# Kernel tuning notes

Measured on AMD Instinct MI355X. Metric: run time of the kernel, lower is better.

The kernel has to match this reference:

```python
import jax, jax.numpy as jnp
import numpy as np

B, N, D_IMG = 64, 196, 2048
T = 32
V, E, H, A = 32000, 512, 1024, 256
PAD_ID = 0


def setup_inputs() -> dict:
    key = jax.random.key(0)
    ks = jax.random.split(key, 16)
    s = lambda *sh: 1.0 / np.sqrt(sh[-1])
    img_seq = jax.random.normal(ks[0], (B, N, D_IMG), dtype=jnp.float32)
    tokens_in = jax.random.randint(ks[1], (B, T), 0, V, dtype=jnp.int64)
    embed = jax.random.normal(ks[2], (V, E), dtype=jnp.float32) * 0.02
    embed = embed.at[PAD_ID].set(0.0)  # padding_idx row is zero
    W_head1 = jax.random.normal(ks[3], (E, E + D_IMG), dtype=jnp.float32) * s(E + D_IMG)
    W_ih = jax.random.normal(ks[4], (4 * H, E), dtype=jnp.float32) * s(H)
    W_hh = jax.random.normal(ks[5], (4 * H, H), dtype=jnp.float32) * s(H)
    b_ih = jax.random.normal(ks[6], (4 * H,), dtype=jnp.float32) * s(H)
    b_hh = jax.random.normal(ks[7], (4 * H,), dtype=jnp.float32) * s(H)
    W_head = jax.random.normal(ks[8], (V, H), dtype=jnp.float32) * s(H)
    W_img = jax.random.normal(ks[9], (A, D_IMG), dtype=jnp.float32) * s(D_IMG)
    W_hid = jax.random.normal(ks[10], (A, H), dtype=jnp.float32) * s(H)
    w_score = jax.random.normal(ks[11], (A,), dtype=jnp.float32) * s(A)
    W_h0 = jax.random.normal(ks[12], (H, D_IMG), dtype=jnp.float32) * s(D_IMG)
    b_h0 = jax.random.normal(ks[13], (H,), dtype=jnp.float32) * s(D_IMG)
    W_c0 = jax.random.normal(ks[14], (H, D_IMG), dtype=jnp.float32) * s(D_IMG)
    b_c0 = jax.random.normal(ks[15], (H,), dtype=jnp.float32) * s(D_IMG)
    return dict(img_seq=img_seq, tokens_in=tokens_in, embed=embed, W_head1=W_head1,
                W_ih=W_ih, W_hh=W_hh, b_ih=b_ih, b_hh=b_hh, W_head=W_head,
                W_img=W_img, W_hid=W_hid, w_score=w_score,
                W_h0=W_h0, b_h0=b_h0, W_c0=W_c0, b_c0=b_c0)


def _decode(img_seq, tokens_in, embed, W_head1, W_ih, W_hh, b_ih, b_hh,
            W_head, W_img, W_hid, w_score, W_h0, b_h0, W_c0, b_c0):
    g = img_seq.mean(axis=1)                              # [B, D]
    h = jnp.tanh(g @ W_h0.T + b_h0)                       # [B, H]
    c = jnp.tanh(g @ W_c0.T + b_c0)                       # [B, H]
    # image projection is time-invariant: hoist out of the loop
    proj_img = jnp.einsum('bnd,ad->bna', img_seq, W_img)  # [B, N, A]
    emb_all = embed[tokens_in]                            # [B, T, E]

    def step(carry, emb_t):
        h, c = carry
        # additive attention
        proj_h = h @ W_hid.T                              # [B, A]
        scores = jnp.einsum('bna,a->bn', jnp.tanh(proj_img + proj_h[:, None, :]), w_score)
        weights = jax.nn.softmax(scores, axis=-1)         # [B, N]
        ctx = jnp.einsum('bn,bnd->bd', weights, img_seq)  # [B, D]
        x = jnp.concatenate([emb_t, ctx], axis=-1) @ W_head1.T  # [B, E]
        # LSTMCell (PyTorch gate order: i, f, g, o)
        gates = x @ W_ih.T + b_ih + h @ W_hh.T + b_hh     # [B, 4H]
        i, f, gg, o = jnp.split(gates, 4, axis=-1)
        c_new = jax.nn.sigmoid(f) * c + jax.nn.sigmoid(i) * jnp.tanh(gg)
        h_new = jax.nn.sigmoid(o) * jnp.tanh(c_new)
        logits = h_new @ W_head.T                         # [B, V]
        return (h_new, c_new), logits

    _, ys = jax.lax.scan(step, (h, c), jnp.swapaxes(emb_all, 0, 1))  # ys: [T, B, V]
    return jnp.swapaxes(ys, 0, 1)                         # [B, T, V]


def reference(img_seq, tokens_in, embed, W_head1, W_ih, W_hh, b_ih, b_hh,
              W_head, W_img, W_hid, w_score, W_h0, b_h0, W_c0, b_c0):
    return _decode(img_seq, tokens_in, embed, W_head1, W_ih, W_hh, b_ih, b_hh,
                   W_head, W_img, W_hid, w_score, W_h0, b_h0, W_c0, b_c0)
```

## Files before the change

kernel.cpp:

```cpp
#include <hip/hip_runtime.h>
#include <stdint.h>

typedef unsigned short u16;
typedef __bf16 bf16x8 __attribute__((ext_vector_type(8)));
typedef float f32x4 __attribute__((ext_vector_type(4)));

#define DEV static __device__ __forceinline__

DEV u16 f2bu(float f) {
    union { float f; unsigned u; } v; v.f = f;
    unsigned r = v.u + 0x7FFFu + ((v.u >> 16) & 1u);
    return (u16)(r >> 16);
}
DEV float b2f(u16 b) {
    union { unsigned u; float f; } v; v.u = ((unsigned)b) << 16;
    return v.f;
}
DEV float fast_tanh(float x) {
    float e = __expf(2.f * x);
    return 1.f - __fdividef(2.f, e + 1.f);
}
DEV float fast_sig(float x) {
    return __fdividef(1.f, 1.f + __expf(-x));
}
DEV void gload_lds(const u16* g, u16* l) {
    __builtin_amdgcn_global_load_lds((const __attribute__((address_space(1))) void*)g,
                                     (__attribute__((address_space(3))) void*)l, 16, 0, 0);
}

template<bool A_F32, bool B_F32, bool B_KXN, bool OUT_BF16, bool BIAS>
__global__ __launch_bounds__(256) void gemm128(
    const void* __restrict__ Ap, int lda,
    const void* __restrict__ Bp, int ldb,
    void* __restrict__ Cp, int ldc,
    const float* __restrict__ bias, int K)
{
    __shared__ u16 As[128 * 40];
    __shared__ u16 Bs[128 * 40];
    const int tid = threadIdx.x;
    const int lane = tid & 63, wave = tid >> 6;
    const int wr = wave >> 1, wc = wave & 1;
    const int m0 = blockIdx.y * 128, n0 = blockIdx.x * 128;

    f32x4 acc[4][4];
#pragma unroll
    for (int m = 0; m < 4; ++m)
#pragma unroll
        for (int n = 0; n < 4; ++n)
            acc[m][n] = (f32x4){0.f, 0.f, 0.f, 0.f};

    for (int k0 = 0; k0 < K; k0 += 32) {
        __syncthreads();
        if (A_F32) {
            const float* A = (const float*)Ap;
#pragma unroll
            for (int i = 0; i < 4; ++i) {
                int c = tid + i * 256;
                int row = c >> 3, kc = (c & 7) * 4;
                float4 v = *(const float4*)&A[(size_t)(m0 + row) * lda + k0 + kc];
                ushort4 o; o.x = f2bu(v.x); o.y = f2bu(v.y); o.z = f2bu(v.z); o.w = f2bu(v.w);
                *(ushort4*)&As[row * 40 + kc] = o;
            }
        } else {
            const u16* A = (const u16*)Ap;
#pragma unroll
            for (int i = 0; i < 2; ++i) {
                int c = tid + i * 256;
                int row = c >> 2, kc = (c & 3) * 8;
                *(int4*)&As[row * 40 + kc] = *(const int4*)&A[(size_t)(m0 + row) * lda + k0 + kc];
            }
        }
        if (B_KXN) {
            const float* B = (const float*)Bp;
#pragma unroll
            for (int i = 0; i < 4; ++i) {
                int c = tid + i * 256;
                int kk = c >> 5, nc = (c & 31) * 4;
                float4 v = *(const float4*)&B[(size_t)(k0 + kk) * ldb + n0 + nc];
                Bs[(nc + 0) * 40 + kk] = f2bu(v.x);
                Bs[(nc + 1) * 40 + kk] = f2bu(v.y);
                Bs[(nc + 2) * 40 + kk] = f2bu(v.z);
                Bs[(nc + 3) * 40 + kk] = f2bu(v.w);
            }
        } else if (B_F32) {
            const float* B = (const float*)Bp;
#pragma unroll
            for (int i = 0; i < 4; ++i) {
                int c = tid + i * 256;
                int row = c >> 3, kc = (c & 7) * 4;
                float4 v = *(const float4*)&B[(size_t)(n0 + row) * ldb + k0 + kc];
                ushort4 o; o.x = f2bu(v.x); o.y = f2bu(v.y); o.z = f2bu(v.z); o.w = f2bu(v.w);
                *(ushort4*)&Bs[row * 40 + kc] = o;
            }
        } else {
            const u16* B = (const u16*)Bp;
#pragma unroll
            for (int i = 0; i < 2; ++i) {
                int c = tid + i * 256;
                int row = c >> 2, kc = (c & 3) * 8;
                *(int4*)&Bs[row * 40 + kc] = *(const int4*)&B[(size_t)(n0 + row) * ldb + k0 + kc];
            }
        }
        __syncthreads();
        const int fr = lane & 15, kq = (lane >> 4) * 8;
        bf16x8 af[4], bq[4];
#pragma unroll
        for (int m = 0; m < 4; ++m)
            af[m] = *(const bf16x8*)&As[(wr * 64 + m * 16 + fr) * 40 + kq];
#pragma unroll
        for (int n = 0; n < 4; ++n)
            bq[n] = *(const bf16x8*)&Bs[(wc * 64 + n * 16 + fr) * 40 + kq];
#pragma unroll
        for (int m = 0; m < 4; ++m)
#pragma unroll
            for (int n = 0; n < 4; ++n)
                acc[m][n] = __builtin_amdgcn_mfma_f32_16x16x32_bf16(af[m], bq[n], acc[m][n], 0, 0, 0);
    }
    const int fr = lane & 15, rq = (lane >> 4) * 4;
#pragma unroll
    for (int m = 0; m < 4; ++m) {
#pragma unroll
        for (int n = 0; n < 4; ++n) {
            int col = n0 + wc * 64 + n * 16 + fr;
            float bv = BIAS ? bias[col] : 0.f;
#pragma unroll
            for (int r = 0; r < 4; ++r) {
                int row = m0 + wr * 64 + m * 16 + rq + r;
                float v = acc[m][n][r] + bv;
                if (OUT_BF16) ((u16*)Cp)[(size_t)row * ldc + col] = f2bu(v);
                else          ((float*)Cp)[(size_t)row * ldc + col] = v;
            }
        }
    }
}

__global__ __launch_bounds__(256) void gemm_head(const u16* __restrict__ A,
                                                 const u16* __restrict__ B,
                                                 float* __restrict__ C)
{
    __shared__ u16 As[128 * 64];
    __shared__ u16 Bs[128 * 64];
    const int tid = threadIdx.x, lane = tid & 63, wave = tid >> 6;
    const int wr = wave >> 1, wc = wave & 1;
    int bid = blockIdx.x;
    int nb = (bid & 7) * 500 + (bid >> 3);
    const int m0 = (nb & 15) * 128;
    const int n0 = (nb >> 4) * 128;

    f32x4 acc[4][4];
#pragma unroll
    for (int m = 0; m < 4; ++m)
#pragma unroll
        for (int n = 0; n < 4; ++n)
            acc[m][n] = (f32x4){0.f, 0.f, 0.f, 0.f};

    const int srg = lane >> 3;
    const int sslot = lane & 7;
    const int fr = lane & 15, kg = lane >> 4;

    for (int k0 = 0; k0 < 1024; k0 += 64) {
        __syncthreads();
#pragma unroll
        for (int j = 0; j < 4; ++j) {
            const int rb = (j * 4 + wave) * 8;
            const int ra = rb + srg;
            const int ge = (sslot ^ (ra & 7)) * 8;
            gload_lds(&A[(size_t)(m0 + ra) * 1024 + k0 + ge], &As[rb * 64]);
            gload_lds(&B[(size_t)(n0 + ra) * 1024 + k0 + ge], &Bs[rb * 64]);
        }
        __syncthreads();
#pragma unroll
        for (int kk = 0; kk < 2; ++kk) {
            const int sl = kk * 4 + kg;
            bf16x8 af[4], bq[4];
#pragma unroll
            for (int m = 0; m < 4; ++m) {
                const int row = wr * 64 + m * 16 + fr;
                af[m] = *(const bf16x8*)&As[row * 64 + ((sl ^ (row & 7)) << 3)];
            }
#pragma unroll
            for (int n = 0; n < 4; ++n) {
                const int row = wc * 64 + n * 16 + fr;
                bq[n] = *(const bf16x8*)&Bs[row * 64 + ((sl ^ (row & 7)) << 3)];
            }
#pragma unroll
            for (int m = 0; m < 4; ++m)
#pragma unroll
                for (int n = 0; n < 4; ++n)
                    acc[m][n] = __builtin_amdgcn_mfma_f32_16x16x32_bf16(af[m], bq[n], acc[m][n], 0, 0, 0);
        }
    }
    const int rq = kg * 4;
#pragma unroll
    for (int m = 0; m < 4; ++m)
#pragma unroll
        for (int n = 0; n < 4; ++n) {
            int col = n0 + wc * 64 + n * 16 + fr;
#pragma unroll
            for (int r = 0; r < 4; ++r)
                C[(size_t)(m0 + wr * 64 + m * 16 + rq + r) * 32000 + col] = acc[m][n][r];
        }
}

__global__ __launch_bounds__(256) void prep_k(
    const float* __restrict__ img, const float* __restrict__ Whh,
    const float* __restrict__ Whid, const float* __restrict__ Whead,
    const int* __restrict__ tok, const float* __restrict__ embed,
    const float* __restrict__ bih, const float* __restrict__ bhh,
    u16* __restrict__ img_bf, u16* __restrict__ Whh_bf,
    u16* __restrict__ Whid_bf, u16* __restrict__ Whead_bf,
    u16* __restrict__ emb_bf, float* __restrict__ bsum)
{
    const int bid = blockIdx.x;
    if (bid < 25088) {
        int i = bid * 256 + threadIdx.x;
        float4 v = ((const float4*)img)[i];
        ushort4 o; o.x = f2bu(v.x); o.y = f2bu(v.y); o.z = f2bu(v.z); o.w = f2bu(v.w);
        ((ushort4*)img_bf)[i] = o;
    } else if (bid < 29184) {
        int i = (bid - 25088) * 256 + threadIdx.x;
        float4 v = ((const float4*)Whh)[i];
        ushort4 o; o.x = f2bu(v.x); o.y = f2bu(v.y); o.z = f2bu(v.z); o.w = f2bu(v.w);
        ((ushort4*)Whh_bf)[i] = o;
    } else if (bid < 29440) {
        int i = (bid - 29184) * 256 + threadIdx.x;
        float4 v = ((const float4*)Whid)[i];
        ushort4 o; o.x = f2bu(v.x); o.y = f2bu(v.y); o.z = f2bu(v.z); o.w = f2bu(v.w);
        ((ushort4*)Whid_bf)[i] = o;
    } else if (bid < 61440) {
        int i = (bid - 29440) * 256 + threadIdx.x;
        float4 v = ((const float4*)Whead)[i];
        ushort4 o; o.x = f2bu(v.x); o.y = f2bu(v.y); o.z = f2bu(v.z); o.w = f2bu(v.w);
        ((ushort4*)Whead_bf)[i] = o;
    } else if (bid < 65536) {
        int id = (bid - 61440) * 256 + threadIdx.x;
        int row = id >> 9, e = id & 511;
        int t = row >> 6, b = row & 63;
        int tk = tok[b * 32 + t];
        emb_bf[(size_t)row * 512 + e] = f2bu(embed[(size_t)tk * 512 + e]);
    } else {
        int i = (bid - 65536) * 256 + threadIdx.x;
        bsum[i] = bih[i] + bhh[i];
    }
}

__global__ __launch_bounds__(256) void pack_w(const u16* __restrict__ Wic,
                                              const u16* __restrict__ Whh,
                                              u16* __restrict__ Wpk)
{
    const int bid = blockIdx.y;
    const int t2 = blockIdx.x * 256 + threadIdx.x;
    const int i = t2 >> 6, lane = t2 & 63;
    const int fr = lane & 15, kq = (lane >> 4) * 8;
    const int grow = ((fr >> 2) << 10) + bid * 4 + (fr & 3);
    const int k0 = i * 32;
    int4 v;
    if (k0 < 2048) v = *(const int4*)&Wic[(size_t)grow * 2048 + k0 + kq];
    else           v = *(const int4*)&Whh[(size_t)grow * 1024 + (k0 - 2048) + kq];
    *(int4*)&Wpk[((size_t)bid * 6144 + t2) * 8] = v;
}

__global__ __launch_bounds__(256) void mean_k(const u16* __restrict__ img_bf, float* __restrict__ gT)
{
    int id = blockIdx.x * 256 + threadIdx.x;
    int b = id >> 10;
    int d = (id & 1023) * 2;
    const u16* base = img_bf + (size_t)b * 196 * 2048 + d;
    float s0 = 0.f, s1 = 0.f;
#pragma unroll 4
    for (int n = 0; n < 196; ++n) {
        ushort2 v = *(const ushort2*)(base + (size_t)n * 2048);
        s0 += b2f(v.x);
        s1 += b2f(v.y);
    }
    gT[(d + 0) * 64 + b] = s0 * (1.f / 196.f);
    gT[(d + 1) * 64 + b] = s1 * (1.f / 196.f);
}

__global__ __launch_bounds__(256) void h0c0(const float* __restrict__ gT,
                                            const float* __restrict__ Wh0, const float* __restrict__ bh0,
                                            const float* __restrict__ Wc0, const float* __restrict__ bc0,
                                            float* __restrict__ c, u16* __restrict__ h0)
{
    int id = blockIdx.x * 256 + threadIdx.x;
    int b = id & 63, n = id >> 6;
    const float4* Wh = (const float4*)&Wh0[(size_t)n * 2048];
    const float4* Wc = (const float4*)&Wc0[(size_t)n * 2048];
    float s0 = 0.f, s1 = 0.f;
#pragma unroll 4
    for (int k4 = 0; k4 < 512; ++k4) {
        float4 wh = Wh[k4], wc = Wc[k4];
        float g0 = gT[(k4 * 4 + 0) * 64 + b];
        float g1 = gT[(k4 * 4 + 1) * 64 + b];
        float g2 = gT[(k4 * 4 + 2) * 64 + b];
        float g3 = gT[(k4 * 4 + 3) * 64 + b];
        s0 += wh.x * g0 + wh.y * g1 + wh.z * g2 + wh.w * g3;
        s1 += wc.x * g0 + wc.y * g1 + wc.z * g2 + wc.w * g3;
    }
    c[b * 1024 + n] = fast_tanh(s1 + bc0[n]);
    h0[(size_t)b * 1024 + n] = f2bu(fast_tanh(s0 + bh0[n]));
}


__global__ __launch_bounds__(512) void ph_k(const u16* __restrict__ hb,
                                            const u16* __restrict__ Whid_bf,
                                            float* __restrict__ ph_all)
{
    const int tid = threadIdx.x, lane = tid & 63, wave = tid >> 6;
    const int fr = lane & 15, kq = (lane >> 4) * 8, rq = (lane >> 4) * 4;
    const int a0 = blockIdx.x * 16;
    __shared__ float red[8][64][16];
    f32x4 acc[4];
#pragma unroll
    for (int m = 0; m < 4; ++m) acc[m] = (f32x4){0.f, 0.f, 0.f, 0.f};
#pragma unroll
    for (int kk = 0; kk < 128; kk += 32) {
        const int k0 = wave * 128 + kk;
        bf16x8 bq = *(const bf16x8*)&Whid_bf[(size_t)(a0 + fr) * 1024 + k0 + kq];
#pragma unroll
        for (int m = 0; m < 4; ++m) {
            bf16x8 af = *(const bf16x8*)&hb[(size_t)(m * 16 + fr) * 1024 + k0 + kq];
            acc[m] = __builtin_amdgcn_mfma_f32_16x16x32_bf16(af, bq, acc[m], 0, 0, 0);
        }
    }
#pragma unroll
    for (int m = 0; m < 4; ++m)
#pragma unroll
        for (int r = 0; r < 4; ++r)
            red[wave][m * 16 + rq + r][fr] = acc[m][r];
    __syncthreads();
#pragma unroll
    for (int i = 0; i < 2; ++i) {
        const int idx = tid + i * 512;
        const int bb = idx >> 4, a = idx & 15;
        float s = 0.f;
#pragma unroll
        for (int w8 = 0; w8 < 8; ++w8) s += red[w8][bb][a];
        ph_all[bb * 256 + a0 + a] = s;
    }
}

__global__ __launch_bounds__(1024) void attn_k(const float* __restrict__ ph_all,
                                               const float* __restrict__ w_score,
                                               const u16* __restrict__ proj_bf,
                                               const u16* __restrict__ img_bf,
                                               u16* __restrict__ ctx_bf)
{
    const int b = blockIdx.x >> 2, q = blockIdx.x & 3;
    const int tid = threadIdx.x, lane = tid & 63, wave = tid >> 6;
    __shared__ float ph[256], ws[256], sc[256], red[256];
    __shared__ float part[16][512];
    if (tid < 256) {
        ph[tid] = ph_all[b * 256 + tid];
        ws[tid] = w_score[tid];
        sc[tid] = -1e30f;
    }
    __syncthreads();
    for (int n = wave; n < 196; n += 16) {
        const int a0 = lane * 4;
        ushort4 pv = *(const ushort4*)&proj_bf[((size_t)b * 196 + n) * 256 + a0];
        float s = ws[a0 + 0] * fast_tanh(b2f(pv.x) + ph[a0 + 0])
                + ws[a0 + 1] * fast_tanh(b2f(pv.y) + ph[a0 + 1])
                + ws[a0 + 2] * fast_tanh(b2f(pv.z) + ph[a0 + 2])
                + ws[a0 + 3] * fast_tanh(b2f(pv.w) + ph[a0 + 3]);
#pragma unroll
        for (int off = 32; off; off >>= 1) s += __shfl_xor(s, off, 64);
        if (lane == 0) sc[n] = s;
    }
    __syncthreads();
    if (tid < 256) red[tid] = sc[tid];
    __syncthreads();
#pragma unroll
    for (int s2 = 128; s2 > 0; s2 >>= 1) {
        if (tid < s2) red[tid] = fmaxf(red[tid], red[tid + s2]);
        __syncthreads();
    }
    const float mx = red[0];
    __syncthreads();
    float e = (tid < 196) ? __expf(sc[tid] - mx) : 0.f;
    if (tid < 256) red[tid] = e;
    __syncthreads();
#pragma unroll
    for (int s2 = 128; s2 > 0; s2 >>= 1) {
        if (tid < s2) red[tid] += red[tid + s2];
        __syncthreads();
    }
    const float inv = __fdividef(1.f, red[0]);
    __syncthreads();
    if (tid < 256) sc[tid] = e * inv;
    __syncthreads();
    const int gid = tid >> 4, st = tid & 15;
    const int c0 = q * 512 + gid * 8;
    const u16* base = img_bf + ((size_t)b * 196) * 2048 + c0;
    float a[8];
#pragma unroll
    for (int i = 0; i < 8; ++i) a[i] = 0.f;
    for (int n = st; n < 196; n += 16) {
        bf16x8 v = *(const bf16x8*)(base + (size_t)n * 2048);
        float wgt = sc[n];
#pragma unroll
        for (int i = 0; i < 8; ++i) a[i] += wgt * (float)v[i];
    }
#pragma unroll
    for (int i = 0; i < 8; ++i) part[st][gid * 8 + i] = a[i];
    __syncthreads();
    if (tid < 512) {
        const int col = tid;
        float v = 0.f;
#pragma unroll
        for (int s16 = 0; s16 < 16; ++s16) v += part[s16][col];
        ctx_bf[(size_t)b * 2048 + q * 512 + col] = f2bu(v);
    }
}

__global__ __launch_bounds__(1024) void gates_k(const u16* __restrict__ ctx_bf,
                                                const u16* __restrict__ hb,
                                                const u16* __restrict__ Wpk,
                                                const float* __restrict__ xg,
                                                float* __restrict__ cbuf,
                                                u16* __restrict__ h_nxt,
                                                u16* __restrict__ h_all,
                                                int t)
{
    const int tid = threadIdx.x, lane = tid & 63, wave = tid >> 6;
    const int fr = lane & 15, kq = (lane >> 4) * 8, rq = (lane >> 4) * 4;
    const int hc0 = blockIdx.x * 4;
    const u16* Wblk = Wpk + (size_t)blockIdx.x * 49152 + lane * 8;
    __shared__ float red[16][64][16];

    f32x4 acc[4];
#pragma unroll
    for (int m = 0; m < 4; ++m) acc[m] = (f32x4){0.f, 0.f, 0.f, 0.f};

    const int kbeg = wave * 192, kend = kbeg + 192;
    const int cend = kend < 2048 ? kend : 2048;
#pragma unroll 2
    for (int k0 = kbeg; k0 < cend; k0 += 32) {
        bf16x8 bq = *(const bf16x8*)&Wblk[(size_t)(k0 >> 5) * 512];
#pragma unroll
        for (int m = 0; m < 4; ++m) {
            bf16x8 af = *(const bf16x8*)&ctx_bf[(size_t)(m * 16 + fr) * 2048 + k0 + kq];
            acc[m] = __builtin_amdgcn_mfma_f32_16x16x32_bf16(af, bq, acc[m], 0, 0, 0);
        }
    }
    const int hbeg = kbeg > 2048 ? kbeg - 2048 : 0;
    const int hend = kend > 2048 ? kend - 2048 : 0;
#pragma unroll 2
    for (int kh = hbeg; kh < hend; kh += 32) {
        bf16x8 bq = *(const bf16x8*)&Wblk[(size_t)((kh + 2048) >> 5) * 512];
#pragma unroll
        for (int m = 0; m < 4; ++m) {
            bf16x8 af = *(const bf16x8*)&hb[(size_t)(m * 16 + fr) * 1024 + kh + kq];
            acc[m] = __builtin_amdgcn_mfma_f32_16x16x32_bf16(af, bq, acc[m], 0, 0, 0);
        }
    }
#pragma unroll
    for (int m = 0; m < 4; ++m)
#pragma unroll
        for (int r = 0; r < 4; ++r)
            red[wave][m * 16 + rq + r][fr] = acc[m][r];
    __syncthreads();

    if (tid < 256) {
        const int bb = tid >> 2, j = tid & 3;
        const int col = hc0 + j;
        float G[4];
#pragma unroll
        for (int g = 0; g < 4; ++g) {
            const int f2 = g * 4 + j;
            float s = 0.f;
#pragma unroll
            for (int w16 = 0; w16 < 16; ++w16) s += red[w16][bb][f2];
            G[g] = s + xg[((size_t)t * 64 + bb) * 4096 + g * 1024 + col];
        }
        float ig = fast_sig(G[0]), fg = fast_sig(G[1]);
        float gv = fast_tanh(G[2]), og = fast_sig(G[3]);
        float cp = cbuf[bb * 1024 + col];
        float cn = fg * cp + ig * gv;
        cbuf[bb * 1024 + col] = cn;
        u16 hv = f2bu(og * fast_tanh(cn));
        h_nxt[(size_t)bb * 1024 + col] = hv;
        h_all[((size_t)bb * 32 + t) * 1024 + col] = hv;
    }
}

extern "C" void kernel_launch(void* const* d_in, const int* in_sizes, int n_in,
                              void* d_out, int out_size, void* d_ws, size_t ws_size,
                              hipStream_t stream)
{
    const float* img     = (const float*)d_in[0];
    const int*   tok     = (const int*)d_in[1];
    const float* embed   = (const float*)d_in[2];
    const float* W_head1 = (const float*)d_in[3];
    const float* W_ih    = (const float*)d_in[4];
    const float* W_hh    = (const float*)d_in[5];
    const float* b_ih    = (const float*)d_in[6];
    const float* b_hh    = (const float*)d_in[7];
    const float* W_head  = (const float*)d_in[8];
    const float* W_img   = (const float*)d_in[9];
    const float* W_hid   = (const float*)d_in[10];
    const float* w_score = (const float*)d_in[11];
    const float* W_h0    = (const float*)d_in[12];
    const float* b_h0    = (const float*)d_in[13];
    const float* W_c0    = (const float*)d_in[14];
    const float* b_c0    = (const float*)d_in[15];
    float* out = (float*)d_out;

    char* w = (char*)d_ws;
    size_t off = 0;
    auto alloc = [&](size_t bytes) { char* p = w + off; off += (bytes + 255) & ~(size_t)255; return p; };

    u16*   Wic      = (u16*)alloc(4096ULL * 2048 * 2);
    u16*   Whh_bf   = (u16*)alloc(4096ULL * 1024 * 2);
    u16*   Wpk      = (u16*)alloc(256ULL * 96 * 64 * 8 * 2);
    u16*   Whid_bf  = (u16*)alloc(256ULL * 1024 * 2);
    u16*   Whead_bf = (u16*)alloc(32000ULL * 1024 * 2);
    u16*   img_bf   = (u16*)alloc(64ULL * 196 * 2048 * 2);
    float* xg       = (float*)alloc(2048ULL * 4096 * 4);
    u16*   proj_bf  = (u16*)alloc(64ULL * 196 * 256 * 2);
    u16*   emb_bf   = (u16*)alloc(2048ULL * 512 * 2);
    u16*   xe       = (u16*)alloc(2048ULL * 512 * 2);
    float* gT       = (float*)alloc(2048ULL * 64 * 4);
    float* cbuf     = (float*)alloc(64ULL * 1024 * 4);
    u16*   hbuf     = (u16*)alloc(2ULL * 64 * 1024 * 2);
    u16*   ctx_bf   = (u16*)alloc(64ULL * 2048 * 2);
    u16*   h_all    = (u16*)alloc(2048ULL * 1024 * 2);
    float* ph_all   = (float*)alloc(64ULL * 256 * 4);
    float* bsum     = (float*)alloc(4096ULL * 4);
    (void)ws_size; (void)in_sizes; (void)n_in; (void)out_size;

    prep_k<<<dim3(65552), dim3(256), 0, stream>>>(img, W_hh, W_hid, W_head, tok, embed,
                                                  b_ih, b_hh, img_bf, Whh_bf, Whid_bf,
                                                  Whead_bf, emb_bf, bsum);
    mean_k<<<dim3(256), dim3(256), 0, stream>>>(img_bf, gT);
    h0c0<<<dim3(256), dim3(256), 0, stream>>>(gT, W_h0, b_h0, W_c0, b_c0, cbuf, hbuf);

    gemm128<false, true, false, true, false><<<dim3(4, 16), dim3(256), 0, stream>>>(
        emb_bf, 512, W_head1, 2560, xe, 512, nullptr, 512);
    gemm128<false, true, false, false, true><<<dim3(32, 16), dim3(256), 0, stream>>>(
        xe, 512, W_ih, 512, xg, 4096, bsum, 512);
    gemm128<true, true, true, true, false><<<dim3(16, 32), dim3(256), 0, stream>>>(
        W_ih, 512, W_head1 + 512, 2560, Wic, 2048, nullptr, 512);
    gemm128<false, true, false, true, false><<<dim3(2, 98), dim3(256), 0, stream>>>(
        img_bf, 2048, W_img, 2048, proj_bf, 256, nullptr, 2048);
    pack_w<<<dim3(24, 256), dim3(256), 0, stream>>>(Wic, Whh_bf, Wpk);

    for (int t = 0; t < 32; ++t) {
        u16* hb = hbuf + (size_t)(t & 1) * 65536;
        u16* hn = hbuf + (size_t)((t + 1) & 1) * 65536;
        ph_k<<<dim3(16), dim3(512), 0, stream>>>(hb, Whid_bf, ph_all);
        attn_k<<<dim3(256), dim3(1024), 0, stream>>>(ph_all, w_score, proj_bf, img_bf, ctx_bf);
        gates_k<<<dim3(256), dim3(1024), 0, stream>>>(ctx_bf, hb, Wpk, xg, cbuf, hn, h_all, t);
    }

    gemm_head<<<dim3(4000), dim3(256), 0, stream>>>(h_all, Whead_bf, out);
}
```

Before: 2.023 ms.

## Fuse hidden-state attention projection into attn_k and widen head GEMM tile

Removes the separate ph_k launch per timestep. Each attention block now recomputes the h·W_hid projection for its own batch row, reading a transposed bf16 W_hid laid out for coalesced 8-wide loads. This saves 32 kernel launches and the ph_all round trip, but the projection is recomputed redundantly in each of the 4 blocks per batch row, using scalar FMAs. Separately, the output-head GEMM moves to 512-thread blocks with a 128x256 tile, halving the grid and reusing A tiles across more columns.

```diff
diff --git a/kernel.cpp b/kernel.cpp
--- a/kernel.cpp
+++ b/kernel.cpp
@@ -134,18 +134,18 @@
     }
 }
 
-__global__ __launch_bounds__(256) void gemm_head(const u16* __restrict__ A,
-                                                 const u16* __restrict__ B,
-                                                 float* __restrict__ C)
+__global__ __launch_bounds__(512, 4) void gemm_head(const u16* __restrict__ A,
+                                                    const u16* __restrict__ B,
+                                                    float* __restrict__ C)
 {
     __shared__ u16 As[128 * 64];
-    __shared__ u16 Bs[128 * 64];
+    __shared__ u16 Bs[256 * 64];
     const int tid = threadIdx.x, lane = tid & 63, wave = tid >> 6;
-    const int wr = wave >> 1, wc = wave & 1;
+    const int wr = wave >> 2, wc = wave & 3;
     int bid = blockIdx.x;
-    int nb = (bid & 7) * 500 + (bid >> 3);
+    int nb = (bid & 7) * 250 + (bid >> 3);
     const int m0 = (nb & 15) * 128;
-    const int n0 = (nb >> 4) * 128;
+    const int n0 = (nb >> 4) * 256;
 
     f32x4 acc[4][4];
 #pragma unroll
@@ -156,17 +156,20 @@
 
     const int srg = lane >> 3;
     const int sslot = lane & 7;
+    const int ge = (sslot ^ srg) * 8;
     const int fr = lane & 15, kg = lane >> 4;
 
     for (int k0 = 0; k0 < 1024; k0 += 64) {
         __syncthreads();
 #pragma unroll
+        for (int j = 0; j < 2; ++j) {
+            const int g = wave * 2 + j;
+            gload_lds(&A[(size_t)(m0 + g * 8 + srg) * 1024 + k0 + ge], &As[g * 8 * 64]);
+        }
+#pragma unroll
         for (int j = 0; j < 4; ++j) {
-            const int rb = (j * 4 + wave) * 8;
-            const int ra = rb + srg;
-            const int ge = (sslot ^ (ra & 7)) * 8;
-            gload_lds(&A[(size_t)(m0 + ra) * 1024 + k0 + ge], &As[rb * 64]);
-            gload_lds(&B[(size_t)(n0 + ra) * 1024 + k0 + ge], &Bs[rb * 64]);
+            const int g = wave * 4 + j;
+            gload_lds(&B[(size_t)(n0 + g * 8 + srg) * 1024 + k0 + ge], &Bs[g * 8 * 64]);
         }
         __syncthreads();
 #pragma unroll
@@ -208,7 +211,7 @@
     const int* __restrict__ tok, const float* __restrict__ embed,
     const float* __restrict__ bih, const float* __restrict__ bhh,
     u16* __restrict__ img_bf, u16* __restrict__ Whh_bf,
-    u16* __restrict__ Whid_bf, u16* __restrict__ Whead_bf,
+    u16* __restrict__ WhidT, u16* __restrict__ Whead_bf,
     u16* __restrict__ emb_bf, float* __restrict__ bsum)
 {
     const int bid = blockIdx.x;
@@ -224,9 +227,10 @@
         ((ushort4*)Whh_bf)[i] = o;
     } else if (bid < 29440) {
         int i = (bid - 29184) * 256 + threadIdx.x;
-        float4 v = ((const float4*)Whid)[i];
+        int a = i >> 8, k4 = (i & 255) * 4;
+        float4 v = *(const float4*)&Whid[(size_t)a * 1024 + k4];
         ushort4 o; o.x = f2bu(v.x); o.y = f2bu(v.y); o.z = f2bu(v.z); o.w = f2bu(v.w);
-        ((ushort4*)Whid_bf)[i] = o;
+        *(ushort4*)&WhidT[(size_t)(k4 >> 3) * 2048 + a * 8 + (k4 & 7)] = o;
     } else if (bid < 61440) {
         int i = (bid - 29440) * 256 + threadIdx.x;
         float4 v = ((const float4*)Whead)[i];
@@ -301,46 +305,8 @@
     h0[(size_t)b * 1024 + n] = f2bu(fast_tanh(s0 + bh0[n]));
 }
 
-
-__global__ __launch_bounds__(512) void ph_k(const u16* __restrict__ hb,
-                                            const u16* __restrict__ Whid_bf,
-                                            float* __restrict__ ph_all)
-{
-    const int tid = threadIdx.x, lane = tid & 63, wave = tid >> 6;
-    const int fr = lane & 15, kq = (lane >> 4) * 8, rq = (lane >> 4) * 4;
-    const int a0 = blockIdx.x * 16;
-    __shared__ float red[8][64][16];
-    f32x4 acc[4];
-#pragma unroll
-    for (int m = 0; m < 4; ++m) acc[m] = (f32x4){0.f, 0.f, 0.f, 0.f};
-#pragma unroll
-    for (int kk = 0; kk < 128; kk += 32) {
-        const int k0 = wave * 128 + kk;
-        bf16x8 bq = *(const bf16x8*)&Whid_bf[(size_t)(a0 + fr) * 1024 + k0 + kq];
-#pragma unroll
-        for (int m = 0; m < 4; ++m) {
-            bf16x8 af = *(const bf16x8*)&hb[(size_t)(m * 16 + fr) * 1024 + k0 + kq];
-            acc[m] = __builtin_amdgcn_mfma_f32_16x16x32_bf16(af, bq, acc[m], 0, 0, 0);
-        }
-    }
-#pragma unroll
-    for (int m = 0; m < 4; ++m)
-#pragma unroll
-        for (int r = 0; r < 4; ++r)
-            red[wave][m * 16 + rq + r][fr] = acc[m][r];
-    __syncthreads();
-#pragma unroll
-    for (int i = 0; i < 2; ++i) {
-        const int idx = tid + i * 512;
-        const int bb = idx >> 4, a = idx & 15;
-        float s = 0.f;
-#pragma unroll
-        for (int w8 = 0; w8 < 8; ++w8) s += red[w8][bb][a];
-        ph_all[bb * 256 + a0 + a] = s;
-    }
-}
-
-__global__ __launch_bounds__(1024) void attn_k(const float* __restrict__ ph_all,
+__global__ __launch_bounds__(1024) void attn_k(const u16* __restrict__ hb,
+                                               const u16* __restrict__ WhidT,
                                                const float* __restrict__ w_score,
                                                const u16* __restrict__ proj_bf,
                                                const u16* __restrict__ img_bf,
@@ -349,13 +315,35 @@
     const int b = blockIdx.x >> 2, q = blockIdx.x & 3;
     const int tid = threadIdx.x, lane = tid & 63, wave = tid >> 6;
     __shared__ float ph[256], ws[256], sc[256], red[256];
+    __shared__ float hsh[1024];
+    __shared__ float php[4][256];
     __shared__ float part[16][512];
+
     if (tid < 256) {
-        ph[tid] = ph_all[b * 256 + tid];
         ws[tid] = w_score[tid];
         sc[tid] = -1e30f;
     }
-    __syncthreads();
+    hsh[tid] = b2f(hb[(size_t)b * 1024 + tid]);
+    __syncthreads();
+
+    {
+        const int a = tid & 255, ks = tid >> 8;
+        float s = 0.f;
+        const u16* wp = WhidT + a * 8;
+#pragma unroll 8
+        for (int j = 0; j < 32; ++j) {
+            const int kb = ks * 32 + j;
+            bf16x8 wv = *(const bf16x8*)(wp + (size_t)kb * 2048);
+            const float* hk = &hsh[kb * 8];
+#pragma unroll
+            for (int i = 0; i < 8; ++i) s += hk[i] * (float)wv[i];
+        }
+        php[ks][a] = s;
+    }
+    __syncthreads();
+    if (tid < 256) ph[tid] = php[0][tid] + php[1][tid] + php[2][tid] + php[3][tid];
+    __syncthreads();
+
     for (int n = wave; n < 196; n += 16) {
         const int a0 = lane * 4;
         ushort4 pv = *(const ushort4*)&proj_bf[((size_t)b * 196 + n) * 256 + a0];
@@ -513,7 +501,7 @@
     u16*   Wic      = (u16*)alloc(4096ULL * 2048 * 2);
     u16*   Whh_bf   = (u16*)alloc(4096ULL * 1024 * 2);
     u16*   Wpk      = (u16*)alloc(256ULL * 96 * 64 * 8 * 2);
-    u16*   Whid_bf  = (u16*)alloc(256ULL * 1024 * 2);
+    u16*   WhidT    = (u16*)alloc(256ULL * 1024 * 2);
     u16*   Whead_bf = (u16*)alloc(32000ULL * 1024 * 2);
     u16*   img_bf   = (u16*)alloc(64ULL * 196 * 2048 * 2);
     float* xg       = (float*)alloc(2048ULL * 4096 * 4);
@@ -525,12 +513,11 @@
     u16*   hbuf     = (u16*)alloc(2ULL * 64 * 1024 * 2);
     u16*   ctx_bf   = (u16*)alloc(64ULL * 2048 * 2);
     u16*   h_all    = (u16*)alloc(2048ULL * 1024 * 2);
-    float* ph_all   = (float*)alloc(64ULL * 256 * 4);
     float* bsum     = (float*)alloc(4096ULL * 4);
     (void)ws_size; (void)in_sizes; (void)n_in; (void)out_size;
 
     prep_k<<<dim3(65552), dim3(256), 0, stream>>>(img, W_hh, W_hid, W_head, tok, embed,
-                                                  b_ih, b_hh, img_bf, Whh_bf, Whid_bf,
+                                                  b_ih, b_hh, img_bf, Whh_bf, WhidT,
                                                   Whead_bf, emb_bf, bsum);
     mean_k<<<dim3(256), dim3(256), 0, stream>>>(img_bf, gT);
     h0c0<<<dim3(256), dim3(256), 0, stream>>>(gT, W_h0, b_h0, W_c0, b_c0, cbuf, hbuf);
@@ -548,10 +535,9 @@
     for (int t = 0; t < 32; ++t) {
         u16* hb = hbuf + (size_t)(t & 1) * 65536;
         u16* hn = hbuf + (size_t)((t + 1) & 1) * 65536;
-        ph_k<<<dim3(16), dim3(512), 0, stream>>>(hb, Whid_bf, ph_all);
-        attn_k<<<dim3(256), dim3(1024), 0, stream>>>(ph_all, w_score, proj_bf, img_bf, ctx_bf);
+        attn_k<<<dim3(256), dim3(1024), 0, stream>>>(hb, WhidT, w_score, proj_bf, img_bf, ctx_bf);
         gates_k<<<dim3(256), dim3(1024), 0, stream>>>(ctx_bf, hb, Wpk, xg, cbuf, hn, h_all, t);
     }
 
-    gemm_head<<<dim3(4000), dim3(256), 0, stream>>>(h_all, Whead_bf, out);
-}
+    gemm_head<<<dim3(2000), dim3(512), 0, stream>>>(h_all, Whead_bf, out);
+}
```

New measurement: 1.941 ms. -4.0%, faster.
